# Kernel tuning notes

Measured on AMD Instinct MI355X. Metric: run time of the kernel, lower is better.

Reference implementation:

```python
import jax, jax.numpy as jnp
import numpy as np

B, T, D_EMB, D_QKV = 8, 2048, 1024, 64
SCALE = 1.0 / (D_QKV ** 0.5)


def setup_inputs() -> dict:
    key = jax.random.key(0)
    kx, kq, kk, kv = jax.random.split(key, 4)
    return {
        "x": jax.random.normal(kx, (B, T, D_EMB), dtype=jnp.float32),
        "Wq": jax.random.normal(kq, (D_EMB, D_QKV), dtype=jnp.float32) * 0.02,
        "Wk": jax.random.normal(kk, (D_EMB, D_QKV), dtype=jnp.float32) * 0.02,
        "Wv": jax.random.normal(kv, (D_EMB, D_QKV), dtype=jnp.float32) * 0.02,
    }


def reference(x, Wq, Wk, Wv):
    # x: [B, T, D_emb]; projections to [B, T, D_qkv]
    q = jnp.einsum("bte,ed->btd", x, Wq)
    k = jnp.einsum("bte,ed->btd", x, Wk)
    v = jnp.einsum("bte,ed->btd", x, Wv)
    # scores: [B, T, T], scaled then causally masked
    scores = jnp.einsum("bqd,bkd->bqk", q, k) * SCALE
    t = x.shape[1]
    causal = jnp.tril(jnp.ones((t, t), dtype=bool))
    scores = jnp.where(causal[None, :, :], scores, -jnp.inf)
    attn = jax.nn.softmax(scores, axis=-1)
    return jnp.einsum("bqk,bkd->bqd", attn, v)
```

## Files before the change

kernel.cpp:

```cpp
#include <hip/hip_runtime.h>

typedef float f32x4 __attribute__((ext_vector_type(4)));
typedef __bf16 bf16x8 __attribute__((ext_vector_type(8)));
typedef __bf16 bf16x4 __attribute__((ext_vector_type(4)));

#define T_ 2048
#define DE 1024
#define DQ 64
#define SCALE 0.125f

#define GL16(gp, lp)                                                        \
  __builtin_amdgcn_global_load_lds(                                         \
      (const __attribute__((address_space(1))) void*)(gp),                  \
      (__attribute__((address_space(3))) void*)(lp), 16, 0, 0)

#define WAITVM(N) asm volatile("s_waitcnt vmcnt(" #N ")" ::: "memory")

__global__ __launch_bounds__(256) void kw_pack(
    const float* __restrict__ Wq, const float* __restrict__ Wk,
    const float* __restrict__ Wv, __bf16* __restrict__ Wf)
{
  int tid = blockIdx.x * 256 + threadIdx.x;
  int lane = tid & 63, f = tid >> 6;
  int t = f % 12, kc = f / 12;
  const float* W = (t < 4) ? Wq : ((t < 8) ? Wk : Wv);
  int nl = (t & 3) * 16 + (lane & 15);
  int k0 = kc * 32 + (lane >> 4) * 8;
  bf16x8 v;
#pragma unroll
  for (int j = 0; j < 8; ++j) v[j] = (__bf16)W[(size_t)(k0 + j) * 64 + nl];
  *(bf16x8*)(Wf + (size_t)tid * 8) = v;
}

__global__ __launch_bounds__(256) void kproj(
    const float* __restrict__ x, const __bf16* __restrict__ Wf,
    __bf16* __restrict__ Qb, __bf16* __restrict__ Kb, __bf16* __restrict__ Vt)
{
  __shared__ char lds[3 * 8192 + 2 * 24576];
  const int tid = threadIdx.x;
  const int lane = tid & 63;
  const int w = tid >> 6;
  const int col = lane & 15, g = lane >> 4;
  const int msub = w & 1;
  const int ng = w >> 1;
  const int mbase = blockIdx.x * 32;

  size_t gsrcA[2];
  int ldstA[2];
#pragma unroll
  for (int cc = 0; cc < 2; ++cc) {
    int q = w * 2 + cc;
    int row = q * 4 + (lane >> 4);
    int kbyte = ((lane & 15) * 16) ^ ((row & 7) << 4);
    gsrcA[cc] = (size_t)(mbase + row) * 4096 + (size_t)kbyte;
    ldstA[cc] = q * 1024 + lane * 16;
  }
  int ofsB[6];
#pragma unroll
  for (int cc = 0; cc < 6; ++cc) ofsB[cc] = (w * 6 + cc) * 1024 + lane * 16;

  f32x4 acc[6];
#pragma unroll
  for (int i = 0; i < 6; ++i) acc[i] = (f32x4){0.f, 0.f, 0.f, 0.f};

  const char* xb = (const char*)x;
  const char* wb = (const char*)Wf;

#define STAGE_A(ks)                                                         \
  {                                                                         \
    char* lb = &lds[((ks) % 3) * 8192];                                     \
    _Pragma("unroll")                                                       \
    for (int cc = 0; cc < 2; ++cc)                                          \
      GL16(xb + gsrcA[cc] + (size_t)(ks) * 256, lb + ldstA[cc]);            \
  }
#define STAGE_B(ks)                                                         \
  {                                                                         \
    char* lb = &lds[24576 + ((ks) & 1) * 24576];                            \
    _Pragma("unroll")                                                       \
    for (int cc = 0; cc < 6; ++cc)                                          \
      GL16(wb + (size_t)(ks) * 24576 + ofsB[cc], lb + ofsB[cc]);            \
  }
#define KSTEP(ks)                                                           \
  {                                                                         \
    const char* la = &lds[((ks) % 3) * 8192];                               \
    const char* lbB = &lds[24576 + ((ks) & 1) * 24576];                     \
    const int arow = msub * 16 + col;                                       \
    const char* abase = la + arow * 256;                                    \
    const int sw = (arow & 7) << 4;                                         \
    _Pragma("unroll")                                                       \
    for (int kh = 0; kh < 2; ++kh) {                                        \
      int kb = kh * 128 + g * 32;                                           \
      f32x4 a0 = *(const f32x4*)(abase + (kb ^ sw));                        \
      f32x4 a1 = *(const f32x4*)(abase + ((kb + 16) ^ sw));                 \
      bf16x8 af;                                                            \
      _Pragma("unroll")                                                     \
      for (int j = 0; j < 4; ++j) { af[j] = (__bf16)a0[j]; af[4 + j] = (__bf16)a1[j]; } \
      _Pragma("unroll")                                                     \
      for (int ii = 0; ii < 6; ++ii) {                                      \
        int nt = ng * 6 + ii;                                               \
        bf16x8 bfr = *(const bf16x8*)(lbB + ((kh * 12 + nt) * 64 + lane) * 16); \
        acc[ii] = __builtin_amdgcn_mfma_f32_16x16x32_bf16(af, bfr, acc[ii], 0, 0, 0); \
      }                                                                     \
    }                                                                       \
  }
#define ITER(ks, vm, doB, doA)                                              \
  WAITVM(vm);                                                               \
  __builtin_amdgcn_s_barrier();                                             \
  __builtin_amdgcn_sched_barrier(0);                                        \
  if (doB) STAGE_B((ks) + 1);                                               \
  if (doA) STAGE_A((ks) + 2);                                               \
  KSTEP(ks);

  STAGE_A(0);
  STAGE_B(0);
  STAGE_A(1);

  ITER(0, 2, 1, 1)  ITER(1, 2, 1, 1)  ITER(2, 2, 1, 1)  ITER(3, 2, 1, 1)
  ITER(4, 2, 1, 1)  ITER(5, 2, 1, 1)  ITER(6, 2, 1, 1)  ITER(7, 2, 1, 1)
  ITER(8, 2, 1, 1)  ITER(9, 2, 1, 1)  ITER(10, 2, 1, 1) ITER(11, 2, 1, 1)
  ITER(12, 2, 1, 1) ITER(13, 2, 1, 1) ITER(14, 2, 1, 0) ITER(15, 0, 0, 0)

#undef ITER
#undef KSTEP
#undef STAGE_B
#undef STAGE_A

  const int b = mbase >> 11;
  const int mrow = mbase + msub * 16 + g * 4;
  const int trow = (mbase & 2047) + msub * 16 + g * 4;
#pragma unroll
  for (int ii = 0; ii < 6; ++ii) {
    int ti = ng * 6 + ii;
    if (ti < 8) {
      __bf16* dst = (ti < 4) ? Qb : Kb;
      int c = (ti & 3) * 16 + col;
#pragma unroll
      for (int r = 0; r < 4; ++r)
        dst[(size_t)(mrow + r) * DQ + c] = (__bf16)acc[ii][r];
    } else {
      int d = (ti - 8) * 16 + col;
      bf16x4 v;
#pragma unroll
      for (int r = 0; r < 4; ++r) v[r] = (__bf16)acc[ii][r];
      *(bf16x4*)(Vt + ((size_t)(b * DQ + d)) * T_ + trow) = v;
    }
  }
}

__global__ __launch_bounds__(256) void kattn(
    const __bf16* __restrict__ Qb, const __bf16* __restrict__ Kb,
    const __bf16* __restrict__ Vt, float* __restrict__ out)
{
  __shared__ float accs[4][32][68];
  __shared__ float mls[4][2][32];
  __shared__ __bf16 plds[4][2][16][72];

  const int tid = threadIdx.x;
  const int lane = tid & 63;
  const int w = tid >> 6;
  const int col = lane & 15, g = lane >> 4;
  const int b = blockIdx.x & 7;
  const int jq = 63 - (blockIdx.x >> 3);
  const int qbase = jq * 32;

  bf16x8 qa[2][2];
#pragma unroll
  for (int mt = 0; mt < 2; ++mt) {
    const __bf16* Qp = Qb + (size_t)(b * T_ + qbase + mt * 16 + col) * DQ + g * 8;
    qa[mt][0] = *(const bf16x8*)(Qp);
    qa[mt][1] = *(const bf16x8*)(Qp + 32);
  }

  const __bf16* Kbb = Kb + (size_t)b * T_ * DQ;
  const __bf16* Vbb = Vt + (size_t)b * DQ * T_;

  f32x4 acc[2][4];
#pragma unroll
  for (int mt = 0; mt < 2; ++mt)
#pragma unroll
    for (int dt = 0; dt < 4; ++dt) acc[mt][dt] = (f32x4){0.f,0.f,0.f,0.f};
  float mrun[2][4], lsum[2][4];
#pragma unroll
  for (int mt = 0; mt < 2; ++mt)
#pragma unroll
    for (int r = 0; r < 4; ++r) { mrun[mt][r] = -1e30f; lsum[mt][r] = 0.f; }

  const int nb = (jq >> 1) + 1;
  for (int it = w; it < nb; it += 4) {
    const int nbase = it * 64;

    bf16x8 kf_[4][2];
#pragma unroll
    for (int nt = 0; nt < 4; ++nt) {
      const __bf16* Kp = Kbb + (size_t)(nbase + nt * 16 + col) * DQ + g * 8;
      kf_[nt][0] = *(const bf16x8*)(Kp);
      kf_[nt][1] = *(const bf16x8*)(Kp + 32);
    }

    f32x4 s[2][4];
#pragma unroll
    for (int mt = 0; mt < 2; ++mt)
#pragma unroll
      for (int nt = 0; nt < 4; ++nt) {
        f32x4 t = __builtin_amdgcn_mfma_f32_16x16x32_bf16(qa[mt][0], kf_[nt][0],
                                                          (f32x4){0.f,0.f,0.f,0.f}, 0, 0, 0);
        s[mt][nt] = __builtin_amdgcn_mfma_f32_16x16x32_bf16(qa[mt][1], kf_[nt][1], t, 0, 0, 0);
      }

    bf16x8 vf[4][2];
#pragma unroll
    for (int dt = 0; dt < 4; ++dt) {
      const __bf16* Vp = Vbb + (size_t)(dt * 16 + col) * T_ + nbase + g * 8;
      vf[dt][0] = *(const bf16x8*)(Vp);
      vf[dt][1] = *(const bf16x8*)(Vp + 32);
    }

#pragma unroll
    for (int mt = 0; mt < 2; ++mt)
#pragma unroll
      for (int nt = 0; nt < 4; ++nt)
#pragma unroll
        for (int r = 0; r < 4; ++r) s[mt][nt][r] *= SCALE;
    if (it == nb - 1) {
#pragma unroll
      for (int mt = 0; mt < 2; ++mt)
#pragma unroll
        for (int nt = 0; nt < 4; ++nt)
#pragma unroll
          for (int r = 0; r < 4; ++r)
            if (nbase + nt * 16 + col > qbase + mt * 16 + g * 4 + r) s[mt][nt][r] = -1e30f;
    }

    float mv[2][4];
#pragma unroll
    for (int mt = 0; mt < 2; ++mt)
#pragma unroll
      for (int r = 0; r < 4; ++r)
        mv[mt][r] = fmaxf(fmaxf(s[mt][0][r], s[mt][1][r]), fmaxf(s[mt][2][r], s[mt][3][r]));
#pragma unroll
    for (int sh = 1; sh <= 8; sh <<= 1)
#pragma unroll
      for (int mt = 0; mt < 2; ++mt)
#pragma unroll
        for (int r = 0; r < 4; ++r) mv[mt][r] = fmaxf(mv[mt][r], __shfl_xor(mv[mt][r], sh, 64));

#pragma unroll
    for (int mt = 0; mt < 2; ++mt)
#pragma unroll
      for (int r = 0; r < 4; ++r) {
        float mn = fmaxf(mrun[mt][r], mv[mt][r]);
        float rs = __expf(mrun[mt][r] - mn);
        mrun[mt][r] = mn;
        float ps = 0.f;
#pragma unroll
        for (int nt = 0; nt < 4; ++nt) {
          s[mt][nt][r] = __expf(s[mt][nt][r] - mn);
          ps += s[mt][nt][r];
        }
        lsum[mt][r] = lsum[mt][r] * rs + ps;
#pragma unroll
        for (int dt = 0; dt < 4; ++dt) acc[mt][dt][r] *= rs;
      }

#pragma unroll
    for (int mt = 0; mt < 2; ++mt)
#pragma unroll
      for (int nt = 0; nt < 4; ++nt)
#pragma unroll
        for (int r = 0; r < 4; ++r)
          plds[w][mt][g * 4 + r][nt * 16 + col] = (__bf16)s[mt][nt][r];

    bf16x8 pa[2][2];
#pragma unroll
    for (int mt = 0; mt < 2; ++mt) {
      pa[mt][0] = *(const bf16x8*)&plds[w][mt][col][g * 8];
      pa[mt][1] = *(const bf16x8*)&plds[w][mt][col][32 + g * 8];
    }

#pragma unroll
    for (int mt = 0; mt < 2; ++mt)
#pragma unroll
      for (int dt = 0; dt < 4; ++dt) {
        f32x4 t = __builtin_amdgcn_mfma_f32_16x16x32_bf16(pa[mt][0], vf[dt][0], acc[mt][dt], 0, 0, 0);
        acc[mt][dt] = __builtin_amdgcn_mfma_f32_16x16x32_bf16(pa[mt][1], vf[dt][1], t, 0, 0, 0);
      }
  }

#pragma unroll
  for (int sh = 1; sh <= 8; sh <<= 1)
#pragma unroll
    for (int mt = 0; mt < 2; ++mt)
#pragma unroll
      for (int r = 0; r < 4; ++r) lsum[mt][r] += __shfl_xor(lsum[mt][r], sh, 64);

#pragma unroll
  for (int mt = 0; mt < 2; ++mt)
#pragma unroll
    for (int r = 0; r < 4; ++r) {
      int row = mt * 16 + g * 4 + r;
      accs[w][row][col]      = acc[mt][0][r];
      accs[w][row][col + 16] = acc[mt][1][r];
      accs[w][row][col + 32] = acc[mt][2][r];
      accs[w][row][col + 48] = acc[mt][3][r];
      if (col == 0) { mls[w][0][row] = mrun[mt][r]; mls[w][1][row] = lsum[mt][r]; }
    }
  __syncthreads();

#pragma unroll
  for (int pass = 0; pass < 2; ++pass) {
    int row = pass * 16 + (tid >> 4);
    int c4 = (tid & 15) * 4;
    float m0 = mls[0][0][row], m1 = mls[1][0][row];
    float m2 = mls[2][0][row], m3 = mls[3][0][row];
    float M = fmaxf(fmaxf(m0, m1), fmaxf(m2, m3));
    float s0 = __expf(m0 - M), s1 = __expf(m1 - M);
    float s2 = __expf(m2 - M), s3 = __expf(m3 - M);
    float L = s0 * mls[0][1][row] + s1 * mls[1][1][row]
            + s2 * mls[2][1][row] + s3 * mls[3][1][row];
    f32x4 a0 = *(const f32x4*)&accs[0][row][c4];
    f32x4 a1 = *(const f32x4*)&accs[1][row][c4];
    f32x4 a2 = *(const f32x4*)&accs[2][row][c4];
    f32x4 a3 = *(const f32x4*)&accs[3][row][c4];
    float inv = 1.f / L;
    f32x4 o;
#pragma unroll
    for (int j = 0; j < 4; ++j)
      o[j] = (s0 * a0[j] + s1 * a1[j] + s2 * a2[j] + s3 * a3[j]) * inv;
    *(f32x4*)(out + (size_t)(b * T_ + qbase + row) * DQ + c4) = o;
  }
}

extern "C" void kernel_launch(void* const* d_in, const int* in_sizes, int n_in,
                              void* d_out, int out_size, void* d_ws, size_t ws_size,
                              hipStream_t stream)
{
  const float* x  = (const float*)d_in[0];
  const float* Wq = (const float*)d_in[1];
  const float* Wk = (const float*)d_in[2];
  const float* Wv = (const float*)d_in[3];
  float* out = (float*)d_out;

  char* ws = (char*)d_ws;
  __bf16* Wf = (__bf16*)(ws);
  __bf16* Qb = (__bf16*)(ws + 0x80000);
  __bf16* Kb = (__bf16*)(ws + 0x80000 + 0x200000);
  __bf16* Vt = (__bf16*)(ws + 0x80000 + 0x400000);

  kw_pack<<<96, 256, 0, stream>>>(Wq, Wk, Wv, Wf);
  kproj<<<512, 256, 0, stream>>>(x, Wf, Qb, Kb, Vt);
  kattn<<<512, 256, 0, stream>>>(Qb, Kb, Vt, out);
}
```

Before: 50.94 us.

## Prefetch K tiles into swizzled LDS via async loads and skip softmax rescale

Each wave now stages its next K tile into a per-wave XOR-swizzled LDS buffer with global_load_lds, issued right after the current tile is read, so K fetch latency overlaps compute. V loads are hoisted ahead of the QK MFMAs. The online softmax skips the max reduction and accumulator rescale when no row's new max exceeds the running max by more than 8, which removes shuffles and exp work at the cost of trusting that the stale max keeps exp values bounded. LDS is repacked into one aliased buffer, with the K buffers reused for the final accumulator merge.

Result: faster. 47.45 us (-6.9%).

```diff
diff --git a/kernel.cpp b/kernel.cpp
--- a/kernel.cpp
+++ b/kernel.cpp
@@ -151,10 +151,7 @@
     const __bf16* __restrict__ Qb, const __bf16* __restrict__ Kb,
     const __bf16* __restrict__ Vt, float* __restrict__ out)
 {
-  __shared__ float accs[4][32][68];
-  __shared__ float mls[4][2][32];
-  __shared__ __bf16 plds[4][2][16][72];
-
+  __shared__ char smem[54272];
   const int tid = threadIdx.x;
   const int lane = tid & 63;
   const int w = tid >> 6;
@@ -163,6 +160,10 @@
   const int jq = 63 - (blockIdx.x >> 3);
   const int qbase = jq * 32;
 
+  char* kbuf = smem + w * 8704;
+  __bf16* pld = (__bf16*)(smem + 34816 + w * 4608);
+  float* mls = (float*)(smem + 53248);
+
   bf16x8 qa[2][2];
 #pragma unroll
   for (int mt = 0; mt < 2; ++mt) {
@@ -171,8 +172,18 @@
     qa[mt][1] = *(const bf16x8*)(Qp + 32);
   }
 
-  const __bf16* Kbb = Kb + (size_t)b * T_ * DQ;
+  const char* Kbb = (const char*)(Kb + (size_t)b * T_ * DQ);
   const __bf16* Vbb = Vt + (size_t)b * DQ * T_;
+
+  size_t gofK[8];
+  int lofK[8];
+#pragma unroll
+  for (int c = 0; c < 8; ++c) {
+    int o = (c * 64 + lane) * 16;
+    int row = o >> 7, slot = (o >> 4) & 7;
+    lofK[c] = o;
+    gofK[c] = (size_t)row * 128 + (size_t)((slot * 16) ^ ((row & 7) << 4));
+  }
 
   f32x4 acc[2][4];
 #pragma unroll
@@ -186,15 +197,43 @@
     for (int r = 0; r < 4; ++r) { mrun[mt][r] = -1e30f; lsum[mt][r] = 0.f; }
 
   const int nb = (jq >> 1) + 1;
+
+  if (w < nb) {
+    const char* src = Kbb + (size_t)(w * 64) * 128;
+#pragma unroll
+    for (int c = 0; c < 8; ++c) GL16(src + gofK[c], kbuf + lofK[c]);
+  }
+  WAITVM(0);
+  __builtin_amdgcn_sched_barrier(0);
+
   for (int it = w; it < nb; it += 4) {
     const int nbase = it * 64;
 
     bf16x8 kf_[4][2];
 #pragma unroll
-    for (int nt = 0; nt < 4; ++nt) {
-      const __bf16* Kp = Kbb + (size_t)(nbase + nt * 16 + col) * DQ + g * 8;
-      kf_[nt][0] = *(const bf16x8*)(Kp);
-      kf_[nt][1] = *(const bf16x8*)(Kp + 32);
+    for (int nt = 0; nt < 4; ++nt)
+#pragma unroll
+      for (int h = 0; h < 2; ++h) {
+        int krow = nt * 16 + col;
+        int bo = krow * 128 + ((h * 64 + g * 16) ^ ((krow & 7) << 4));
+        kf_[nt][h] = *(const bf16x8*)(kbuf + bo);
+      }
+    asm volatile("s_waitcnt lgkmcnt(0)" ::: "memory");
+    __builtin_amdgcn_sched_barrier(0);
+
+    if (it + 4 < nb) {
+      const char* src = Kbb + (size_t)((it + 4) * 64) * 128;
+#pragma unroll
+      for (int c = 0; c < 8; ++c) GL16(src + gofK[c], kbuf + lofK[c]);
+    }
+    __builtin_amdgcn_sched_barrier(0);
+
+    bf16x8 vf[4][2];
+#pragma unroll
+    for (int dt = 0; dt < 4; ++dt) {
+      const __bf16* Vp = Vbb + (size_t)(dt * 16 + col) * T_ + nbase + g * 8;
+      vf[dt][0] = *(const bf16x8*)(Vp);
+      vf[dt][1] = *(const bf16x8*)(Vp + 32);
     }
 
     f32x4 s[2][4];
@@ -207,14 +246,6 @@
         s[mt][nt] = __builtin_amdgcn_mfma_f32_16x16x32_bf16(qa[mt][1], kf_[nt][1], t, 0, 0, 0);
       }
 
-    bf16x8 vf[4][2];
-#pragma unroll
-    for (int dt = 0; dt < 4; ++dt) {
-      const __bf16* Vp = Vbb + (size_t)(dt * 16 + col) * T_ + nbase + g * 8;
-      vf[dt][0] = *(const bf16x8*)(Vp);
-      vf[dt][1] = *(const bf16x8*)(Vp + 32);
-    }
-
 #pragma unroll
     for (int mt = 0; mt < 2; ++mt)
 #pragma unroll
@@ -231,36 +262,62 @@
             if (nbase + nt * 16 + col > qbase + mt * 16 + g * 4 + r) s[mt][nt][r] = -1e30f;
     }
 
-    float mv[2][4];
+    float pmax[2][4];
 #pragma unroll
     for (int mt = 0; mt < 2; ++mt)
 #pragma unroll
       for (int r = 0; r < 4; ++r)
-        mv[mt][r] = fmaxf(fmaxf(s[mt][0][r], s[mt][1][r]), fmaxf(s[mt][2][r], s[mt][3][r]));
-#pragma unroll
-    for (int sh = 1; sh <= 8; sh <<= 1)
+        pmax[mt][r] = fmaxf(fmaxf(s[mt][0][r], s[mt][1][r]), fmaxf(s[mt][2][r], s[mt][3][r]));
+    bool need = false;
+#pragma unroll
+    for (int mt = 0; mt < 2; ++mt)
+#pragma unroll
+      for (int r = 0; r < 4; ++r)
+        need = need || (pmax[mt][r] > mrun[mt][r] + 8.f);
+
+    if (__any(need)) {
+      float mv[2][4];
 #pragma unroll
       for (int mt = 0; mt < 2; ++mt)
 #pragma unroll
-        for (int r = 0; r < 4; ++r) mv[mt][r] = fmaxf(mv[mt][r], __shfl_xor(mv[mt][r], sh, 64));
-
-#pragma unroll
-    for (int mt = 0; mt < 2; ++mt)
-#pragma unroll
-      for (int r = 0; r < 4; ++r) {
-        float mn = fmaxf(mrun[mt][r], mv[mt][r]);
-        float rs = __expf(mrun[mt][r] - mn);
-        mrun[mt][r] = mn;
-        float ps = 0.f;
-#pragma unroll
-        for (int nt = 0; nt < 4; ++nt) {
-          s[mt][nt][r] = __expf(s[mt][nt][r] - mn);
-          ps += s[mt][nt][r];
+        for (int r = 0; r < 4; ++r) mv[mt][r] = pmax[mt][r];
+#pragma unroll
+      for (int sh = 1; sh <= 8; sh <<= 1)
+#pragma unroll
+        for (int mt = 0; mt < 2; ++mt)
+#pragma unroll
+          for (int r = 0; r < 4; ++r) mv[mt][r] = fmaxf(mv[mt][r], __shfl_xor(mv[mt][r], sh, 64));
+#pragma unroll
+      for (int mt = 0; mt < 2; ++mt)
+#pragma unroll
+        for (int r = 0; r < 4; ++r) {
+          float mn = fmaxf(mrun[mt][r], mv[mt][r]);
+          float rs = __expf(mrun[mt][r] - mn);
+          mrun[mt][r] = mn;
+          float ps = 0.f;
+#pragma unroll
+          for (int nt = 0; nt < 4; ++nt) {
+            s[mt][nt][r] = __expf(s[mt][nt][r] - mn);
+            ps += s[mt][nt][r];
+          }
+          lsum[mt][r] = lsum[mt][r] * rs + ps;
+#pragma unroll
+          for (int dt = 0; dt < 4; ++dt) acc[mt][dt][r] *= rs;
         }
-        lsum[mt][r] = lsum[mt][r] * rs + ps;
-#pragma unroll
-        for (int dt = 0; dt < 4; ++dt) acc[mt][dt][r] *= rs;
-      }
+    } else {
+#pragma unroll
+      for (int mt = 0; mt < 2; ++mt)
+#pragma unroll
+        for (int r = 0; r < 4; ++r) {
+          float ps = 0.f;
+#pragma unroll
+          for (int nt = 0; nt < 4; ++nt) {
+            s[mt][nt][r] = __expf(s[mt][nt][r] - mrun[mt][r]);
+            ps += s[mt][nt][r];
+          }
+          lsum[mt][r] += ps;
+        }
+    }
 
 #pragma unroll
     for (int mt = 0; mt < 2; ++mt)
@@ -268,13 +325,13 @@
       for (int nt = 0; nt < 4; ++nt)
 #pragma unroll
         for (int r = 0; r < 4; ++r)
-          plds[w][mt][g * 4 + r][nt * 16 + col] = (__bf16)s[mt][nt][r];
+          pld[(mt * 16 + g * 4 + r) * 72 + nt * 16 + col] = (__bf16)s[mt][nt][r];
 
     bf16x8 pa[2][2];
 #pragma unroll
     for (int mt = 0; mt < 2; ++mt) {
-      pa[mt][0] = *(const bf16x8*)&plds[w][mt][col][g * 8];
-      pa[mt][1] = *(const bf16x8*)&plds[w][mt][col][32 + g * 8];
+      pa[mt][0] = *(const bf16x8*)&pld[(mt * 16 + col) * 72 + g * 8];
+      pa[mt][1] = *(const bf16x8*)&pld[(mt * 16 + col) * 72 + 32 + g * 8];
     }
 
 #pragma unroll
@@ -293,16 +350,17 @@
 #pragma unroll
       for (int r = 0; r < 4; ++r) lsum[mt][r] += __shfl_xor(lsum[mt][r], sh, 64);
 
+  float* accw = (float*)(smem + w * 8704);
 #pragma unroll
   for (int mt = 0; mt < 2; ++mt)
 #pragma unroll
     for (int r = 0; r < 4; ++r) {
       int row = mt * 16 + g * 4 + r;
-      accs[w][row][col]      = acc[mt][0][r];
-      accs[w][row][col + 16] = acc[mt][1][r];
-      accs[w][row][col + 32] = acc[mt][2][r];
-      accs[w][row][col + 48] = acc[mt][3][r];
-      if (col == 0) { mls[w][0][row] = mrun[mt][r]; mls[w][1][row] = lsum[mt][r]; }
+      accw[row * 68 + col]      = acc[mt][0][r];
+      accw[row * 68 + col + 16] = acc[mt][1][r];
+      accw[row * 68 + col + 32] = acc[mt][2][r];
+      accw[row * 68 + col + 48] = acc[mt][3][r];
+      if (col == 0) { mls[(w * 2 + 0) * 32 + row] = mrun[mt][r]; mls[(w * 2 + 1) * 32 + row] = lsum[mt][r]; }
     }
   __syncthreads();
 
@@ -310,17 +368,17 @@
   for (int pass = 0; pass < 2; ++pass) {
     int row = pass * 16 + (tid >> 4);
     int c4 = (tid & 15) * 4;
-    float m0 = mls[0][0][row], m1 = mls[1][0][row];
-    float m2 = mls[2][0][row], m3 = mls[3][0][row];
+    float m0 = mls[0 * 32 + row], m1 = mls[2 * 32 + row];
+    float m2 = mls[4 * 32 + row], m3 = mls[6 * 32 + row];
     float M = fmaxf(fmaxf(m0, m1), fmaxf(m2, m3));
     float s0 = __expf(m0 - M), s1 = __expf(m1 - M);
     float s2 = __expf(m2 - M), s3 = __expf(m3 - M);
-    float L = s0 * mls[0][1][row] + s1 * mls[1][1][row]
-            + s2 * mls[2][1][row] + s3 * mls[3][1][row];
-    f32x4 a0 = *(const f32x4*)&accs[0][row][c4];
-    f32x4 a1 = *(const f32x4*)&accs[1][row][c4];
-    f32x4 a2 = *(const f32x4*)&accs[2][row][c4];
-    f32x4 a3 = *(const f32x4*)&accs[3][row][c4];
+    float L = s0 * mls[1 * 32 + row] + s1 * mls[3 * 32 + row]
+            + s2 * mls[5 * 32 + row] + s3 * mls[7 * 32 + row];
+    f32x4 a0 = *(const f32x4*)((float*)(smem + 0 * 8704) + row * 68 + c4);
+    f32x4 a1 = *(const f32x4*)((float*)(smem + 1 * 8704) + row * 68 + c4);
+    f32x4 a2 = *(const f32x4*)((float*)(smem + 2 * 8704) + row * 68 + c4);
+    f32x4 a3 = *(const f32x4*)((float*)(smem + 3 * 8704) + row * 68 + c4);
     float inv = 1.f / L;
     f32x4 o;
 #pragma unroll
```
